# Kernel tuning notes

Hardware: AMD Instinct MI355X
Metric: run time of the kernel (lower is better)

The kernel has to match this reference:

```python
import jax, jax.numpy as jnp
import numpy as np

B, L, H = 32, 1024, 1024  # kv_length must equal hidden_size for the bmm to typecheck


def setup_inputs() -> dict:
    key = jax.random.key(0)
    ks = jax.random.split(key, 9)
    s = 0.02  # small init so tanh does not saturate
    return {
        "query": jax.random.normal(ks[0], (B, L, H), dtype=jnp.float32),
        "key": jax.random.normal(ks[1], (B, L, H), dtype=jnp.float32),
        "value": jax.random.normal(ks[2], (B, L, H), dtype=jnp.float32),
        "w1_w": jax.random.normal(ks[3], (H, H), dtype=jnp.float32) * s,
        "w1_b": jax.random.normal(ks[4], (H,), dtype=jnp.float32) * s,
        "w2_w": jax.random.normal(ks[5], (H, H), dtype=jnp.float32) * s,
        "w2_b": jax.random.normal(ks[6], (H,), dtype=jnp.float32) * s,
        "v_w": jax.random.normal(ks[7], (H, H), dtype=jnp.float32) * s,
        "v_b": jax.random.normal(ks[8], (H,), dtype=jnp.float32) * s,
    }


def reference(query, key, value, w1_w, w1_b, w2_w, w2_b, v_w, v_b):
    # score_fn: v(tanh(w1(query) + w2(value))); `key` is unused (del key in source)
    h = jnp.tanh(jnp.einsum("blh,oh->blo", query, w1_w) + w1_b
                 + jnp.einsum("blh,oh->blo", value, w2_w) + w2_b)  # (B, L, H)
    score = jnp.einsum("blh,oh->blo", h, v_w) + v_b                 # (B, L, H)
    attention_weights = jax.nn.softmax(score, axis=-1)              # (B, L, H)
    # torch.bmm(weights, value): contracts weights' last dim (H) with value's kv dim (==H)
    context_vector = jnp.einsum("blk,bkh->blh", attention_weights, value)
    return (attention_weights, context_vector)
```

## Files before the change

kernel.cpp:

```cpp
#include <hip/hip_runtime.h>
#include <cstdint>

using u16 = unsigned short;
using u32 = unsigned int;
typedef __attribute__((ext_vector_type(4))) float f32x4;
typedef __attribute__((ext_vector_type(8))) short short8;
typedef __attribute__((ext_vector_type(4))) u16 u16x4;
typedef __attribute__((ext_vector_type(8))) u16 u16x8;

__device__ __forceinline__ u16 f2bf(float f) {
  u32 u = __builtin_bit_cast(u32, f);
  u += 0x7FFFu + ((u >> 16) & 1u);
  return (u16)(u >> 16);
}
__device__ __forceinline__ float bf2f(u16 x) {
  return __builtin_bit_cast(float, (u32)x << 16);
}

__device__ __forceinline__ void gload16(const void* g, void* l) {
  __builtin_amdgcn_global_load_lds(
      (const __attribute__((address_space(1))) void*)g,
      (__attribute__((address_space(3))) void*)l, 16, 0, 0);
}

__device__ __forceinline__ float fast_tanh(float x) {
  float ax = fabsf(x);
  float e = __expf(-2.0f * ax);
  float r = (1.0f - e) / (1.0f + e);
  return x < 0.0f ? -r : r;
}

#define SBAR() do { asm volatile("" ::: "memory"); __builtin_amdgcn_s_barrier(); asm volatile("" ::: "memory"); } while (0)

template<int N> __device__ __forceinline__ void vmw() {
  if constexpr (N == 10) asm volatile("s_waitcnt vmcnt(10)" ::: "memory");
  else if constexpr (N == 8) asm volatile("s_waitcnt vmcnt(8)" ::: "memory");
  else if constexpr (N == 6) asm volatile("s_waitcnt vmcnt(6)" ::: "memory");
  else if constexpr (N == 4) asm volatile("s_waitcnt vmcnt(4)" ::: "memory");
  else if constexpr (N == 2) asm volatile("s_waitcnt vmcnt(2)" ::: "memory");
  else if constexpr (N == 0) asm volatile("s_waitcnt vmcnt(0)" ::: "memory");
}

__device__ __forceinline__ int swz(int L) { return L ^ (((L >> 9) & 1) << 5); }

__device__ __forceinline__ void swz_mn256(int bid, int& m0, int& n0) {
  int s = (bid & 7) * 64 + (bid >> 3);
  n0 = (s & 3) << 8;
  m0 = (s >> 2) << 8;
}

__global__ void cvt_ker(const float4* __restrict__ src, u16x4* __restrict__ dst, int n4) {
  int i = blockIdx.x * 256 + threadIdx.x;
  if (i < n4) {
    float4 f = src[i];
    u16x4 o = { f2bf(f.x), f2bf(f.y), f2bf(f.z), f2bf(f.w) };
    dst[i] = o;
  }
}

__device__ __forceinline__ void stage_half(
    const u16* __restrict__ A0, const u16* __restrict__ B0,
    const u16* __restrict__ A1, const u16* __restrict__ B1,
    int half_nt, u16* lds, int j, int m0, int n0, int w, int rc0, int rc1)
{
  int jt = j >> 2, hh = j & 3;
  int kk = hh >> 1, isA = hh & 1;
  const u16* src;
  int kt;
  if (jt < half_nt) { src = isA ? A0 : B0; kt = jt; }
  else              { src = isA ? A1 : B1; kt = jt - half_nt; }
  int base_row = isA ? m0 : n0;
  int koff = kt * 64 + kk * 32;
  u16* dst = lds + ((jt & 1) * 4 + hh) * 8192 + w * 512;
  const u16* g0 = src + (size_t)base_row * 1024 + koff;
  gload16(g0 + rc0, dst);
  gload16(g0 + rc1, dst + 4096);
}

__device__ __forceinline__ void rdB4(short8* d, const u16* lds, int buf, int kk, const int* boff) {
  const char* h = (const char*)(lds + (buf * 4 + kk * 2) * 8192);
  d[0] = *(const short8*)(h + boff[0]);
  d[1] = *(const short8*)(h + boff[1]);
  d[2] = *(const short8*)(h + boff[2]);
  d[3] = *(const short8*)(h + boff[3]);
}
__device__ __forceinline__ void rdA4(short8* d, const u16* lds, int buf, int kk, int mh, const int* aoff) {
  const char* h = (const char*)(lds + (buf * 4 + 1 + kk * 2) * 8192);
  d[0] = *(const short8*)(h + aoff[mh * 4 + 0]);
  d[1] = *(const short8*)(h + aoff[mh * 4 + 1]);
  d[2] = *(const short8*)(h + aoff[mh * 4 + 2]);
  d[3] = *(const short8*)(h + aoff[mh * 4 + 3]);
}

#define MFMA16(AS, BS, BASE) do {                                                   \
  __builtin_amdgcn_s_setprio(1);                                                    \
  _Pragma("unroll")                                                                 \
  for (int ni_ = 0; ni_ < 4; ni_++) {                                               \
    acc[(BASE)+0][ni_] = __builtin_amdgcn_mfma_f32_16x16x32_bf16(AS[0], BS[ni_], acc[(BASE)+0][ni_], 0, 0, 0); \
    acc[(BASE)+1][ni_] = __builtin_amdgcn_mfma_f32_16x16x32_bf16(AS[1], BS[ni_], acc[(BASE)+1][ni_], 0, 0, 0); \
    acc[(BASE)+2][ni_] = __builtin_amdgcn_mfma_f32_16x16x32_bf16(AS[2], BS[ni_], acc[(BASE)+2][ni_], 0, 0, 0); \
    acc[(BASE)+3][ni_] = __builtin_amdgcn_mfma_f32_16x16x32_bf16(AS[3], BS[ni_], acc[(BASE)+3][ni_], 0, 0, 0); \
  }                                                                                 \
  __builtin_amdgcn_s_setprio(0);                                                    \
} while (0)

#define TILE(T, V0, V1, V2, V3, S0_, S1_, S2_, S3_, NX) do {                        \
  const int buf_ = (T) & 1;                                                         \
                            \
  rdA4(a1s, lds, buf_, 0, 1, aoff);                                                 \
  if (S0_) stage_half(A0, B0, A1, B1, half_nt, lds, 4 * (T) + 7, m0, n0, w, rc0, rc1); \
  MFMA16(a0s, b0s, 0);                                                              \
  vmw<V0>(); SBAR();                                                                \
               \
  rdB4(b1s, lds, buf_, 1, boff);                                                    \
  rdA4(a0s, lds, buf_, 1, 0, aoff);                                                 \
  if (S1_) stage_half(A0, B0, A1, B1, half_nt, lds, 4 * (T) + 8, m0, n0, w, rc0, rc1); \
  MFMA16(a1s, b0s, 4);                                                              \
  vmw<V1>(); SBAR();                                                                \
                            \
  rdA4(a1s, lds, buf_, 1, 1, aoff);                                                 \
  if (S2_) stage_half(A0, B0, A1, B1, half_nt, lds, 4 * (T) + 9, m0, n0, w, rc0, rc1); \
  MFMA16(a0s, b1s, 0);                                                              \
  vmw<V2>(); SBAR();                                                                \
   \
  if (NX) { rdB4(b0s, lds, buf_ ^ 1, 0, boff); rdA4(a0s, lds, buf_ ^ 1, 0, 0, aoff); } \
  if (S3_) stage_half(A0, B0, A1, B1, half_nt, lds, 4 * (T) + 10, m0, n0, w, rc0, rc1); \
  MFMA16(a1s, b1s, 4);                                                              \
  vmw<V3>(); SBAR();                                                                \
} while (0)

__device__ __forceinline__ void gemm_loop(
    const u16* __restrict__ A0, const u16* __restrict__ B0,
    const u16* __restrict__ A1, const u16* __restrict__ B1,
    int half_nt, int NT, int m0, int n0, u16* lds, f32x4 acc[8][4])
{
  const int tid = threadIdx.x;
  const int w = tid >> 6, lane = tid & 63;
  const int wr = w >> 2, wc = w & 3;
  const int lr = lane & 15, g = lane >> 4;

  int rc0, rc1;
  {
    int seg0 = w * 64 + lane, seg1 = 512 + w * 64 + lane;
    int L0 = swz(seg0 * 16), L1 = swz(seg1 * 16);
    rc0 = (L0 >> 6) * 1024 + ((L0 & 63) >> 1);
    rc1 = (L1 >> 6) * 1024 + ((L1 & 63) >> 1);
  }
  int aoff[8], boff[4];
  #pragma unroll
  for (int mi = 0; mi < 8; mi++)
    aoff[mi] = swz((wr * 128 + mi * 16 + lr) * 64 + g * 16);
  #pragma unroll
  for (int ni = 0; ni < 4; ni++)
    boff[ni] = swz((wc * 64 + ni * 16 + lr) * 64 + g * 16);

  short8 a0s[4], a1s[4], b0s[4], b1s[4];

  #pragma unroll
  for (int j = 0; j < 7; j++)
    stage_half(A0, B0, A1, B1, half_nt, lds, j, m0, n0, w, rc0, rc1);
  vmw<10>();
  SBAR();
  rdB4(b0s, lds, 0, 0, boff);
  rdA4(a0s, lds, 0, 0, 0, aoff);

  for (int t = 0; t < NT - 2; t += 2) {
    TILE(t,     8, 8, 8, 8, 1, 1, 1, 1, true);
    TILE(t + 1, 8, 8, 8, 8, 1, 1, 1, 1, true);
  }
  TILE(NT - 2, 8, 8, 4, 4, 1, 0, 0, 0, true);
  TILE(NT - 1, 0, 0, -1, -1, 0, 0, 0, 0, false);
}

__global__ void __launch_bounds__(512, 2)
gemm1_ker(const u16* __restrict__ q, const u16* __restrict__ v,
          const u16* __restrict__ w1, const u16* __restrict__ w2,
          const float* __restrict__ b1, const float* __restrict__ b2,
          u16* __restrict__ H)
{
  __shared__ u16 lds[65536];
  int m0, n0;
  swz_mn256(blockIdx.x, m0, n0);
  f32x4 acc[8][4];
  #pragma unroll
  for (int mi = 0; mi < 8; mi++)
    #pragma unroll
    for (int ni = 0; ni < 4; ni++) acc[mi][ni] = (f32x4){0.f, 0.f, 0.f, 0.f};

  gemm_loop(q, w1, v, w2, 16, 32, m0, n0, lds, acc);

  int tid = threadIdx.x, w = tid >> 6, lane = tid & 63;
  int wr = w >> 2, wc = w & 3, lr = lane & 15, g = lane >> 4;
  #pragma unroll
  for (int ni = 0; ni < 4; ni++) {
    int col = n0 + wc * 64 + ni * 16 + lr;
    float bias = b1[col] + b2[col];
    #pragma unroll
    for (int mi = 0; mi < 8; mi++)
      #pragma unroll
      for (int r = 0; r < 4; r++) {
        int row = m0 + wr * 128 + mi * 16 + g * 4 + r;
        H[(size_t)row * 1024 + col] = f2bf(fast_tanh(acc[mi][ni][r] + bias));
      }
  }
}

__global__ void __launch_bounds__(512, 2)
escore_ker(const u16* __restrict__ h, const u16* __restrict__ vw,
           const float* __restrict__ vb, u16* __restrict__ E,
           float* __restrict__ partial)
{
  __shared__ u16 lds[65536];
  int m0, n0;
  swz_mn256(blockIdx.x, m0, n0);
  f32x4 acc[8][4];
  #pragma unroll
  for (int mi = 0; mi < 8; mi++)
    #pragma unroll
    for (int ni = 0; ni < 4; ni++) acc[mi][ni] = (f32x4){0.f, 0.f, 0.f, 0.f};

  gemm_loop(h, vw, h, vw, 16, 16, m0, n0, lds, acc);

  int tid = threadIdx.x, w = tid >> 6, lane = tid & 63;
  int wr = w >> 2, wc = w & 3, lr = lane & 15, g = lane >> 4;

  #pragma unroll
  for (int ni = 0; ni < 4; ni++) {
    float vbc = vb[n0 + wc * 64 + ni * 16 + lr];
    #pragma unroll
    for (int mi = 0; mi < 8; mi++)
      #pragma unroll
      for (int r = 0; r < 4; r++)
        acc[mi][ni][r] = __expf(acc[mi][ni][r] + vbc);
  }

  __syncthreads();
  float* ps = (float*)lds;
  #pragma unroll
  for (int mi = 0; mi < 8; mi++) {
    #pragma unroll
    for (int r = 0; r < 4; r++) {
      float t = acc[mi][0][r] + acc[mi][1][r] + acc[mi][2][r] + acc[mi][3][r];
      t += __shfl_xor(t, 1, 64);
      t += __shfl_xor(t, 2, 64);
      t += __shfl_xor(t, 4, 64);
      t += __shfl_xor(t, 8, 64);
      if (lr == 0) ps[wc * 256 + wr * 128 + mi * 16 + g * 4 + r] = t;
    }
  }
  __syncthreads();
  if (tid < 256) {
    float s = ps[tid] + ps[256 + tid] + ps[512 + tid] + ps[768 + tid];
    partial[(size_t)(n0 >> 8) * 32768 + m0 + tid] = s;
  }

  #pragma unroll
  for (int ni = 0; ni < 4; ni++) {
    int col = n0 + wc * 64 + ni * 16 + lr;
    #pragma unroll
    for (int mi = 0; mi < 8; mi++)
      #pragma unroll
      for (int r = 0; r < 4; r++) {
        int row = m0 + wr * 128 + mi * 16 + g * 4 + r;
        E[(size_t)row * 1024 + col] = f2bf(acc[mi][ni][r]);
      }
  }
}

__global__ void rowsum_ker(const float* __restrict__ partial, float* __restrict__ inv) {
  int r = blockIdx.x * 256 + threadIdx.x;
  float s = partial[r] + partial[32768 + r] + partial[65536 + r] + partial[98304 + r];
  inv[r] = 1.0f / s;
}

__global__ void wout_ker(const u16* __restrict__ E, const float* __restrict__ inv,
                         float* __restrict__ out) {
  int t = blockIdx.x * 256 + threadIdx.x;
  size_t base = (size_t)t * 8;
  float sc = inv[t >> 7];
  u16x8 v = *(const u16x8*)(E + base);
  float4 o0, o1;
  o0.x = bf2f(v[0]) * sc; o0.y = bf2f(v[1]) * sc; o0.z = bf2f(v[2]) * sc; o0.w = bf2f(v[3]) * sc;
  o1.x = bf2f(v[4]) * sc; o1.y = bf2f(v[5]) * sc; o1.z = bf2f(v[6]) * sc; o1.w = bf2f(v[7]) * sc;
  *(float4*)(out + base) = o0;
  *(float4*)(out + base + 4) = o1;
}

__global__ void transpose_ker(const u16* __restrict__ in, u16* __restrict__ out) {
  __shared__ u16 tile[64][68];
  int b = blockIdx.z;
  int h0 = blockIdx.x * 64, l0 = blockIdx.y * 64;
  const u16* src = in + (size_t)b * 1048576;
  u16* dst = out + (size_t)b * 1048576;
  int t = threadIdx.x;
  #pragma unroll
  for (int i = 0; i < 4; i++) {
    int idx = i * 1024 + t * 4;
    int r = idx >> 6, c = idx & 63;
    *(u16x4*)&tile[r][c] = *(const u16x4*)&src[(size_t)(l0 + r) * 1024 + h0 + c];
  }
  __syncthreads();
  #pragma unroll
  for (int i = 0; i < 4; i++) {
    int idx = i * 1024 + t * 4;
    int hr = idx >> 6, lc = idx & 63;
    u16x4 val = { tile[lc][hr], tile[lc + 1][hr], tile[lc + 2][hr], tile[lc + 3][hr] };
    *(u16x4*)&dst[(size_t)(h0 + hr) * 1024 + l0 + lc] = val;
  }
}

__global__ void __launch_bounds__(512, 2)
gemm3_ker(const u16* __restrict__ E, const u16* __restrict__ vT,
          const float* __restrict__ inv, float* __restrict__ ctx)
{
  __shared__ u16 lds[65536];
  int m0, n0;
  swz_mn256(blockIdx.x, m0, n0);
  const u16* Bb = vT + (size_t)(m0 >> 10) * 1048576;
  f32x4 acc[8][4];
  #pragma unroll
  for (int mi = 0; mi < 8; mi++)
    #pragma unroll
    for (int ni = 0; ni < 4; ni++) acc[mi][ni] = (f32x4){0.f, 0.f, 0.f, 0.f};

  gemm_loop(E, Bb, E, Bb, 16, 16, m0, n0, lds, acc);

  int tid = threadIdx.x, w = tid >> 6, lane = tid & 63;
  int wr = w >> 2, wc = w & 3, lr = lane & 15, g = lane >> 4;
  #pragma unroll
  for (int mi = 0; mi < 8; mi++) {
    #pragma unroll
    for (int r = 0; r < 4; r++) {
      int row = m0 + wr * 128 + mi * 16 + g * 4 + r;
      float sc = inv[row];
      #pragma unroll
      for (int ni = 0; ni < 4; ni++) {
        int col = n0 + wc * 64 + ni * 16 + lr;
        ctx[(size_t)row * 1024 + col] = acc[mi][ni][r] * sc;
      }
    }
  }
}

extern "C" void kernel_launch(void* const* d_in, const int* in_sizes, int n_in,
                              void* d_out, int out_size, void* d_ws, size_t ws_size,
                              hipStream_t stream) {
  const float* q   = (const float*)d_in[0];
  const float* v   = (const float*)d_in[2];
  const float* w1w = (const float*)d_in[3];
  const float* b1  = (const float*)d_in[4];
  const float* w2w = (const float*)d_in[5];
  const float* b2  = (const float*)d_in[6];
  const float* vww = (const float*)d_in[7];
  const float* vb  = (const float*)d_in[8];

  float* out_w = (float*)d_out;
  float* out_c = out_w + (size_t)33554432;

  u16* q_bf  = (u16*)d_ws;
  u16* v_bf  = q_bf + 33554432;
  u16* h_bf  = v_bf + 33554432;
  u16* w1_bf = h_bf + 33554432;
  u16* w2_bf = w1_bf + 1048576;
  u16* vw_bf = w2_bf + 1048576;
  u16* wsm_bf = q_bf;
  u16* vT_bf  = h_bf;
  float* partial = (float*)w1_bf;
  float* invp    = (float*)w2_bf;

  if (ws_size < (size_t)207618048) return;

  cvt_ker<<<32768, 256, 0, stream>>>((const float4*)q,   (u16x4*)q_bf,  8388608);
  cvt_ker<<<32768, 256, 0, stream>>>((const float4*)v,   (u16x4*)v_bf,  8388608);
  cvt_ker<<<1024,  256, 0, stream>>>((const float4*)w1w, (u16x4*)w1_bf, 262144);
  cvt_ker<<<1024,  256, 0, stream>>>((const float4*)w2w, (u16x4*)w2_bf, 262144);
  cvt_ker<<<1024,  256, 0, stream>>>((const float4*)vww, (u16x4*)vw_bf, 262144);

  gemm1_ker<<<512, 512, 0, stream>>>(q_bf, v_bf, w1_bf, w2_bf, b1, b2, h_bf);
  escore_ker<<<512, 512, 0, stream>>>(h_bf, vw_bf, vb, wsm_bf, partial);
  rowsum_ker<<<128, 256, 0, stream>>>(partial, invp);
  transpose_ker<<<dim3(16, 16, 32), 256, 0, stream>>>(v_bf, vT_bf);
  wout_ker<<<16384, 256, 0, stream>>>(wsm_bf, invp, out_w);
  gemm3_ker<<<512, 512, 0, stream>>>(wsm_bf, vT_bf, invp, out_c);
}
```

Before: 455.9 us.

## Fuse value conversion with transpose, merge weight casts, retune GEMM waitcounts

Adds a kernel that converts value to bf16 and writes both the row-major copy and its transpose in one pass, used when the workspace is large enough, which removes the separate transpose kernel and a re-read of v_bf. The three weight conversions are merged into one launch. The GEMM main loop's vmcnt waits are reshaped so each tile waits once instead of four times, giving loads more overlap with compute but relying on correct counting across stage_half calls. Whether the fused path runs depends on the workspace size the harness provides.

```diff
diff --git a/kernel.cpp b/kernel.cpp
--- a/kernel.cpp
+++ b/kernel.cpp
@@ -55,6 +55,50 @@
     float4 f = src[i];
     u16x4 o = { f2bf(f.x), f2bf(f.y), f2bf(f.z), f2bf(f.w) };
     dst[i] = o;
+  }
+}
+
+__global__ void wcvt_ker(const float4* __restrict__ w1, const float4* __restrict__ w2,
+                         const float4* __restrict__ vw, u16x4* __restrict__ d1,
+                         u16x4* __restrict__ d2, u16x4* __restrict__ d3) {
+  int i = blockIdx.x * 256 + threadIdx.x;
+  const float4* s = blockIdx.y == 0 ? w1 : blockIdx.y == 1 ? w2 : vw;
+  u16x4* d = blockIdx.y == 0 ? d1 : blockIdx.y == 1 ? d2 : d3;
+  float4 f = s[i];
+  u16x4 o = { f2bf(f.x), f2bf(f.y), f2bf(f.z), f2bf(f.w) };
+  d[i] = o;
+}
+
+__global__ void vcvtT_ker(const float* __restrict__ src, u16* __restrict__ v_bf,
+                          u16* __restrict__ vT) {
+  __shared__ u16 tile[64][68];
+  int b = blockIdx.z;
+  int h0 = blockIdx.x * 64, l0 = blockIdx.y * 64;
+  const float* s = src + (size_t)b * 1048576;
+  u16* dv = v_bf + (size_t)b * 1048576;
+  u16* dt = vT + (size_t)b * 1048576;
+  int t = threadIdx.x;
+  #pragma unroll
+  for (int i = 0; i < 4; i++) {
+    int idx = i * 1024 + t * 4;
+    int r = idx >> 6, c = idx & 63;
+    float4 f = *(const float4*)&s[(size_t)(l0 + r) * 1024 + h0 + c];
+    tile[r][c] = f2bf(f.x); tile[r][c + 1] = f2bf(f.y);
+    tile[r][c + 2] = f2bf(f.z); tile[r][c + 3] = f2bf(f.w);
+  }
+  __syncthreads();
+  #pragma unroll
+  for (int i = 0; i < 4; i++) {
+    int idx = i * 1024 + t * 4;
+    int r = idx >> 6, c = idx & 63;
+    *(u16x4*)&dv[(size_t)(l0 + r) * 1024 + h0 + c] = *(const u16x4*)&tile[r][c];
+  }
+  #pragma unroll
+  for (int i = 0; i < 4; i++) {
+    int idx = i * 1024 + t * 4;
+    int hr = idx >> 6, lc = idx & 63;
+    u16x4 val = { tile[lc][hr], tile[lc + 1][hr], tile[lc + 2][hr], tile[lc + 3][hr] };
+    *(u16x4*)&dt[(size_t)(h0 + hr) * 1024 + l0 + lc] = val;
   }
 }
 
@@ -106,23 +150,19 @@
 
 #define TILE(T, V0, V1, V2, V3, S0_, S1_, S2_, S3_, NX) do {                        \
   const int buf_ = (T) & 1;                                                         \
-                            \
   rdA4(a1s, lds, buf_, 0, 1, aoff);                                                 \
   if (S0_) stage_half(A0, B0, A1, B1, half_nt, lds, 4 * (T) + 7, m0, n0, w, rc0, rc1); \
   MFMA16(a0s, b0s, 0);                                                              \
   vmw<V0>(); SBAR();                                                                \
-               \
   rdB4(b1s, lds, buf_, 1, boff);                                                    \
   rdA4(a0s, lds, buf_, 1, 0, aoff);                                                 \
   if (S1_) stage_half(A0, B0, A1, B1, half_nt, lds, 4 * (T) + 8, m0, n0, w, rc0, rc1); \
   MFMA16(a1s, b0s, 4);                                                              \
   vmw<V1>(); SBAR();                                                                \
-                            \
   rdA4(a1s, lds, buf_, 1, 1, aoff);                                                 \
   if (S2_) stage_half(A0, B0, A1, B1, half_nt, lds, 4 * (T) + 9, m0, n0, w, rc0, rc1); \
   MFMA16(a0s, b1s, 0);                                                              \
   vmw<V2>(); SBAR();                                                                \
-   \
   if (NX) { rdB4(b0s, lds, buf_ ^ 1, 0, boff); rdA4(a0s, lds, buf_ ^ 1, 0, 0, aoff); } \
   if (S3_) stage_half(A0, B0, A1, B1, half_nt, lds, 4 * (T) + 10, m0, n0, w, rc0, rc1); \
   MFMA16(a1s, b1s, 4);                                                              \
@@ -164,12 +204,11 @@
   rdB4(b0s, lds, 0, 0, boff);
   rdA4(a0s, lds, 0, 0, 0, aoff);
 
-  for (int t = 0; t < NT - 2; t += 2) {
-    TILE(t,     8, 8, 8, 8, 1, 1, 1, 1, true);
-    TILE(t + 1, 8, 8, 8, 8, 1, 1, 1, 1, true);
-  }
-  TILE(NT - 2, 8, 8, 4, 4, 1, 0, 0, 0, true);
-  TILE(NT - 1, 0, 0, -1, -1, 0, 0, 0, 0, false);
+  TILE(0, 8, -1, 8, 4, 1, 1, 1, 1, true);
+  for (int t = 1; t < NT - 2; ++t)
+    TILE(t, -1, -1, -1, 4, 1, 1, 1, 1, true);
+  TILE(NT - 2, -1, -1, -1, 0, 1, 0, 0, 0, true);
+  TILE(NT - 1, -1, -1, -1, -1, 0, 0, 0, 0, false);
 }
 
 __global__ void __launch_bounds__(512, 2)
@@ -364,22 +403,30 @@
   u16* w2_bf = w1_bf + 1048576;
   u16* vw_bf = w2_bf + 1048576;
   u16* wsm_bf = q_bf;
-  u16* vT_bf  = h_bf;
   float* partial = (float*)w1_bf;
   float* invp    = (float*)w2_bf;
 
   if (ws_size < (size_t)207618048) return;
 
-  cvt_ker<<<32768, 256, 0, stream>>>((const float4*)q,   (u16x4*)q_bf,  8388608);
-  cvt_ker<<<32768, 256, 0, stream>>>((const float4*)v,   (u16x4*)v_bf,  8388608);
-  cvt_ker<<<1024,  256, 0, stream>>>((const float4*)w1w, (u16x4*)w1_bf, 262144);
-  cvt_ker<<<1024,  256, 0, stream>>>((const float4*)w2w, (u16x4*)w2_bf, 262144);
-  cvt_ker<<<1024,  256, 0, stream>>>((const float4*)vww, (u16x4*)vw_bf, 262144);
+  const bool bigws = ws_size >= (size_t)274726912;
+  u16* vT_big = vw_bf + 1048576;
+  u16* vT_bf  = bigws ? vT_big : h_bf;
+
+  cvt_ker<<<32768, 256, 0, stream>>>((const float4*)q, (u16x4*)q_bf, 8388608);
+  if (bigws) {
+    vcvtT_ker<<<dim3(16, 16, 32), 256, 0, stream>>>(v, v_bf, vT_big);
+  } else {
+    cvt_ker<<<32768, 256, 0, stream>>>((const float4*)v, (u16x4*)v_bf, 8388608);
+  }
+  wcvt_ker<<<dim3(1024, 3), 256, 0, stream>>>(
+      (const float4*)w1w, (const float4*)w2w, (const float4*)vww,
+      (u16x4*)w1_bf, (u16x4*)w2_bf, (u16x4*)vw_bf);
 
   gemm1_ker<<<512, 512, 0, stream>>>(q_bf, v_bf, w1_bf, w2_bf, b1, b2, h_bf);
   escore_ker<<<512, 512, 0, stream>>>(h_bf, vw_bf, vb, wsm_bf, partial);
   rowsum_ker<<<128, 256, 0, stream>>>(partial, invp);
-  transpose_ker<<<dim3(16, 16, 32), 256, 0, stream>>>(v_bf, vT_bf);
+  if (!bigws)
+    transpose_ker<<<dim3(16, 16, 32), 256, 0, stream>>>(v_bf, vT_bf);
   wout_ker<<<16384, 256, 0, stream>>>(wsm_bf, invp, out_w);
   gemm3_ker<<<512, 512, 0, stream>>>(wsm_bf, vT_bf, invp, out_c);
 }
```

Result: faster. 440.5 us (-3.4%).
